# Optimization experiments

Hardware: AMD Instinct MI355X
Metric: run time of the kernel (lower is better)

Reference implementation:

```python
import jax, jax.numpy as jnp
import numpy as np
import math

NEG_INF = -1e9  # large negative used as masked-logit value (pre-scaling, as in the original)


def setup_inputs() -> dict:
    key = jax.random.key(0)
    k1, k2, k3 = jax.random.split(key, 3)
    bs, ql, kl, d = 8, 2048, 2048, 512
    return {
        "query": jax.random.normal(k1, (bs, ql, d), dtype=jnp.float32),
        "key": jax.random.normal(k2, (bs, kl, d), dtype=jnp.float32),
        "value": jax.random.normal(k3, (bs, kl, d), dtype=jnp.float32),
        "use_mask": 1,
        "cell_dim": 512,
    }


def reference(query, key, value, use_mask, cell_dim):
    bs, ql, d = query.shape[0], query.shape[1], value.shape[2]
    kl = key.shape[1]
    # [bs, ql, kl] raw scores
    mm = jnp.einsum("bqd,bkd->bqk", query, key)
    if use_mask:
        # mask positions where key index > query index (strictly future)
        q_idx = jnp.arange(ql)[:, None]
        k_idx = jnp.arange(kl)[None, :]
        mask = (k_idx > q_idx).astype(mm.dtype)  # [ql, kl]
        mm = mm + mask[None, :, :] * NEG_INF
    # log_softmax(...).exp() == softmax, computed stably in one pass
    w = jax.nn.softmax(mm / math.sqrt(cell_dim), axis=2)
    # weighted value aggregation (original broadcasts to [bs,ql,kl,d]; einsum fuses it)
    res = jnp.einsum("bqk,bkd->bqd", w, value)
    return res
```

## Files before the change

kernel.cpp:

```cpp
#include <hip/hip_runtime.h>
#include <math.h>

typedef __bf16 bf16x8 __attribute__((ext_vector_type(8)));
typedef float floatx4 __attribute__((ext_vector_type(4)));
typedef unsigned short ushort8_t __attribute__((ext_vector_type(8)));

#define BSZ 8
#define SEQ 2048
#define DIM 512
#define BKEY 32
#define BQ 128
#define NSLOT 70

__device__ __forceinline__ unsigned short f2bf(float f) {
    unsigned int u = __float_as_uint(f);
    u += 0x7fffu + ((u >> 16) & 1u);
    return (unsigned short)(u >> 16);
}
__device__ __forceinline__ float bf2f(unsigned short s) {
    return __uint_as_float(((unsigned int)s) << 16);
}

#define ASYNC16(g, l) __builtin_amdgcn_global_load_lds( \
    (const __attribute__((address_space(1))) unsigned int*)(g), \
    (__attribute__((address_space(3))) unsigned int*)(l), 16, 0, 0)

__global__ __launch_bounds__(256) void conv_k(const float* __restrict__ K,
                                              unsigned short* __restrict__ Kb) {
    size_t i = ((size_t)blockIdx.x * 256 + threadIdx.x) * 8;
    float4 a = *(const float4*)(K + i);
    float4 b = *(const float4*)(K + i + 4);
    ushort8_t u;
    u[0]=f2bf(a.x); u[1]=f2bf(a.y); u[2]=f2bf(a.z); u[3]=f2bf(a.w);
    u[4]=f2bf(b.x); u[5]=f2bf(b.y); u[6]=f2bf(b.z); u[7]=f2bf(b.w);
    *(ushort8_t*)(Kb + i) = u;
}

__global__ __launch_bounds__(256) void trans_v(const float* __restrict__ V,
                                               unsigned short* __restrict__ Vt) {
    __shared__ unsigned short T[BKEY][DIM + 8];
    const int bid = blockIdx.x;
    const int b = bid & 7, kb = bid >> 3;
    const float* src = V + ((size_t)b * SEQ + (size_t)kb * BKEY) * DIM;
    const int tid = threadIdx.x;
    #pragma unroll
    for (int i = 0; i < 16; ++i) {
        const int idx = i * 256 + tid;
        const int key = idx >> 7;
        const int d = (idx & 127) * 4;
        float4 x = *(const float4*)(src + (size_t)key * DIM + d);
        T[key][d]   = f2bf(x.x);
        T[key][d+1] = f2bf(x.y);
        T[key][d+2] = f2bf(x.z);
        T[key][d+3] = f2bf(x.w);
    }
    __syncthreads();
    unsigned short* dst = Vt + (size_t)(b * (SEQ / BKEY) + kb) * DIM * BKEY;
    #pragma unroll
    for (int i = 0; i < 8; ++i) {
        const int cidx = i * 256 + tid;
        const int d = cidx >> 2;
        const int kc = cidx & 3;
        ushort8_t v;
        #pragma unroll
        for (int k2 = 0; k2 < 8; ++k2) v[k2] = T[kc * 8 + k2][d];
        *(ushort8_t*)(dst + cidx * 8) = v;
    }
}


template <int SPLIT>
__global__ __launch_bounds__(512, 2)
void attn_fwd(const float* __restrict__ Q,
              const unsigned short* __restrict__ Kb,
              const unsigned short* __restrict__ Vt,
              unsigned short* __restrict__ PartO,
              float* __restrict__ Pml,
              float* __restrict__ O)
{
    __shared__ unsigned short Ksh[2][BKEY * DIM];
    __shared__ unsigned short Vsh[2][DIM * BKEY];
    __shared__ unsigned short Psh[8 * 16 * BKEY];

    const int tid  = threadIdx.x;
    const int lane = tid & 63;
    const int wv   = tid >> 6;
    const int ml   = lane & 15;
    const int quad = lane >> 4;

    const int bid = blockIdx.x;
    const int b   = bid & 7;
    const int j   = bid >> 3;
    int t, c;
    if (SPLIT) {
        t = 15; c = j;
        while (true) { const int cnt = (t + 2) >> 1; if (c < cnt) break; c -= cnt; --t; }
    } else { t = 15 - j; c = 0; }
    const int kt0 = c * 8;
    const int nk  = 4 * t + 4;
    const int kt1 = min(kt0 + 8, nk);
    const bool is_split = SPLIT && (t >= 2);
    const int q0 = t * BQ;
    const int kdiag = 4 * t;

    const float* Qb = Q + (size_t)b * SEQ * DIM;
    const unsigned short* Kbb = Kb + (size_t)b * SEQ * DIM;
    const unsigned short* Vtb = Vt + (size_t)b * SEQ * DIM;
    float* Ob = O + (size_t)b * SEQ * DIM;

    bf16x8 qf[16];
    {
        const float* qp = Qb + (size_t)(q0 + wv * 16 + ml) * DIM + quad * 8;
        #pragma unroll
        for (int kc = 0; kc < 16; ++kc) {
            float4 x = *(const float4*)(qp + kc * 32);
            float4 y = *(const float4*)(qp + kc * 32 + 4);
            union { bf16x8 v; unsigned short s[8]; } u;
            u.s[0]=f2bf(x.x); u.s[1]=f2bf(x.y); u.s[2]=f2bf(x.z); u.s[3]=f2bf(x.w);
            u.s[4]=f2bf(y.x); u.s[5]=f2bf(y.y); u.s[6]=f2bf(y.z); u.s[7]=f2bf(y.w);
            qf[kc] = u.v;
        }
    }
    asm volatile("" ::: "memory");

    floatx4 acc[32];
    #pragma unroll
    for (int i = 0; i < 32; ++i) acc[i] = (floatx4){0.f, 0.f, 0.f, 0.f};
    float mrun[4] = {-INFINITY, -INFINITY, -INFINITY, -INFINITY};
    float lrun[4] = {0.f, 0.f, 0.f, 0.f};

    const float CS = 1.4426950408889634f * 0.04419417382415922f;

    #define STAGE_K(buf_, kt_) do { \
        const unsigned short* Kt_ = Kbb + (size_t)(kt_) * (BKEY * DIM); \
        unsigned short* Kd_ = &Ksh[(buf_)][0]; \
        _Pragma("unroll") \
        for (int i_ = 0; i_ < 4; ++i_) { \
            const int ci_  = i_ * 512 + tid; \
            const int row_ = ci_ >> 6; \
            const int ch_  = (ci_ & 63) ^ (row_ & 7); \
            ASYNC16(Kt_ + (size_t)row_ * DIM + ch_ * 8, Kd_ + ci_ * 8); \
        } } while (0)
    #define STAGE_V(buf_, kt_) do { \
        const unsigned short* Vt_ = Vtb + (size_t)(kt_) * (DIM * BKEY); \
        unsigned short* Vd_ = &Vsh[(buf_)][0]; \
        _Pragma("unroll") \
        for (int i_ = 0; i_ < 4; ++i_) { \
            const int ci_ = i_ * 512 + tid; \
            const int d_  = ci_ >> 2; \
            const int kc_ = (ci_ & 3) ^ (d_ & 3); \
            ASYNC16(Vt_ + d_ * BKEY + kc_ * 8, Vd_ + ci_ * 8); \
        } } while (0)

    STAGE_K(0, kt0);
    STAGE_V(0, kt0);
    asm volatile("s_waitcnt vmcnt(4)" ::: "memory");
    __builtin_amdgcn_s_barrier();

    int cur = 0;
    for (int kt = kt0; kt < kt1; ++kt) {
        const int k0 = kt * BKEY;
        const bool havenxt = (kt + 1 < kt1);

        if (havenxt) STAGE_K(cur ^ 1, kt + 1);

        const unsigned short* Ks = &Ksh[cur][0];
        floatx4 s0 = (floatx4){0,0,0,0}, s1 = (floatx4){0,0,0,0};
        floatx4 s0b = (floatx4){0,0,0,0}, s1b = (floatx4){0,0,0,0};
        const int sw = ml & 7;
        __builtin_amdgcn_s_setprio(1);
        #pragma unroll
        for (int kc = 0; kc < 16; kc += 2) {
            const int ch0 = kc * 4 + quad, ch1 = (kc + 1) * 4 + quad;
            bf16x8 a0 = *(bf16x8*)&Ks[ml * DIM + ((ch0 ^ sw) << 3)];
            bf16x8 a1 = *(bf16x8*)&Ks[(16 + ml) * DIM + ((ch0 ^ sw) << 3)];
            bf16x8 b0 = *(bf16x8*)&Ks[ml * DIM + ((ch1 ^ sw) << 3)];
            bf16x8 b1 = *(bf16x8*)&Ks[(16 + ml) * DIM + ((ch1 ^ sw) << 3)];
            s0  = __builtin_amdgcn_mfma_f32_16x16x32_bf16(qf[kc],     a0, s0,  0, 0, 0);
            s1  = __builtin_amdgcn_mfma_f32_16x16x32_bf16(qf[kc],     a1, s1,  0, 0, 0);
            s0b = __builtin_amdgcn_mfma_f32_16x16x32_bf16(qf[kc + 1], b0, s0b, 0, 0, 0);
            s1b = __builtin_amdgcn_mfma_f32_16x16x32_bf16(qf[kc + 1], b1, s1b, 0, 0, 0);
        }
        __builtin_amdgcn_s_setprio(0);
        s0 = s0 + s0b;
        s1 = s1 + s1b;

        float z[2][4], pr[2][4], al[4], rs[4];
        if (kt >= kdiag) {
            #pragma unroll
            for (int r = 0; r < 4; ++r) {
                const int qg = q0 + wv * 16 + quad * 4 + r;
                z[0][r] = (k0 + ml > qg)      ? -INFINITY : s0[r] * CS;
                z[1][r] = (k0 + 16 + ml > qg) ? -INFINITY : s1[r] * CS;
            }
        } else {
            #pragma unroll
            for (int r = 0; r < 4; ++r) { z[0][r] = s0[r] * CS; z[1][r] = s1[r] * CS; }
        }
        #pragma unroll
        for (int r = 0; r < 4; ++r) {
            float v = fmaxf(z[0][r], z[1][r]);
            v = fmaxf(v, __shfl_xor(v, 1, 64));
            v = fmaxf(v, __shfl_xor(v, 2, 64));
            v = fmaxf(v, __shfl_xor(v, 4, 64));
            v = fmaxf(v, __shfl_xor(v, 8, 64));
            const float nm = fmaxf(mrun[r], v);
            al[r]   = __builtin_amdgcn_exp2f(mrun[r] - nm);
            mrun[r] = nm;
        }
        #pragma unroll
        for (int r = 0; r < 4; ++r) {
            pr[0][r] = __builtin_amdgcn_exp2f(z[0][r] - mrun[r]);
            pr[1][r] = __builtin_amdgcn_exp2f(z[1][r] - mrun[r]);
            float s = pr[0][r] + pr[1][r];
            s += __shfl_xor(s, 1, 64);
            s += __shfl_xor(s, 2, 64);
            s += __shfl_xor(s, 4, 64);
            s += __shfl_xor(s, 8, 64);
            rs[r] = s;
        }
        #pragma unroll
        for (int r = 0; r < 4; ++r) lrun[r] = lrun[r] * al[r] + rs[r];

        if (al[0] < 1.f || al[1] < 1.f || al[2] < 1.f || al[3] < 1.f) {
            #pragma unroll
            for (int nt = 0; nt < 32; ++nt) {
                acc[nt][0] *= al[0]; acc[nt][1] *= al[1];
                acc[nt][2] *= al[2]; acc[nt][3] *= al[3];
            }
        }

        unsigned short* Pw = &Psh[wv * (16 * BKEY)];
        #pragma unroll
        for (int nt = 0; nt < 2; ++nt) {
            #pragma unroll
            for (int r = 0; r < 4; ++r) {
                const int row = quad * 4 + r, col = nt * 16 + ml;
                Pw[row * BKEY + ((((col >> 3) ^ (row & 3)) << 3) | (col & 7))] = f2bf(pr[nt][r]);
            }
        }
        asm volatile("s_waitcnt lgkmcnt(0)" ::: "memory");
        bf16x8 pf = *(bf16x8*)&Pw[ml * BKEY + ((quad ^ (ml & 3)) << 3)];

        if (havenxt) { asm volatile("s_waitcnt vmcnt(4)" ::: "memory"); }
        else         { asm volatile("s_waitcnt vmcnt(0)" ::: "memory"); }
        __builtin_amdgcn_s_barrier();

        if (havenxt) STAGE_V(cur ^ 1, kt + 1);

        const unsigned short* Vs = &Vsh[cur][0];
        __builtin_amdgcn_s_setprio(1);
        #pragma unroll
        for (int nt = 0; nt < 32; ++nt) {
            const int drow = nt * 16 + ml;
            bf16x8 vf = *(bf16x8*)&Vs[drow * BKEY + ((quad ^ (drow & 3)) << 3)];
            acc[nt] = __builtin_amdgcn_mfma_f32_16x16x32_bf16(pf, vf, acc[nt], 0, 0, 0);
        }
        __builtin_amdgcn_s_setprio(0);

        if (havenxt) {
            asm volatile("s_waitcnt vmcnt(4)" ::: "memory");
            __builtin_amdgcn_s_barrier();
            cur ^= 1;
        }
    }
    #undef STAGE_K
    #undef STAGE_V

    if (!is_split) {
        float inv[4];
        #pragma unroll
        for (int r = 0; r < 4; ++r) inv[r] = 1.f / lrun[r];
        #pragma unroll
        for (int nt = 0; nt < 32; ++nt) {
            #pragma unroll
            for (int r = 0; r < 4; ++r) {
                const int row = q0 + wv * 16 + quad * 4 + r;
                Ob[(size_t)row * DIM + nt * 16 + ml] = acc[nt][r] * inv[r];
            }
        }
    } else {
        const size_t slot = (size_t)(b * NSLOT + j);
        unsigned short* po = PartO + slot * (BQ * DIM);
        #pragma unroll
        for (int nt = 0; nt < 32; ++nt) {
            #pragma unroll
            for (int r = 0; r < 4; ++r) {
                const int prow = wv * 16 + quad * 4 + r;
                po[prow * DIM + nt * 16 + ml] = f2bf(acc[nt][r]);
            }
        }
        if (ml == 0) {
            #pragma unroll
            for (int r = 0; r < 4; ++r) {
                const int prow = wv * 16 + quad * 4 + r;
                Pml[slot * 256 + prow * 2]     = mrun[r];
                Pml[slot * 256 + prow * 2 + 1] = lrun[r];
            }
        }
    }
}

__global__ __launch_bounds__(256)
void attn_merge(const unsigned short* __restrict__ PartO,
                const float* __restrict__ Pml,
                float* __restrict__ O)
{
    const int bid = blockIdx.x;
    const int b = bid & 7;
    const int u = bid >> 3;
    const int t = 2 + (u >> 2);
    const int rg = u & 3;
    const int nc = (t + 2) >> 1;
    int j0 = 0;
    for (int tp = 15; tp > t; --tp) j0 += (tp + 2) >> 1;

    const int r   = threadIdx.x >> 3;
    const int row = rg * 32 + r;
    const int d0  = (threadIdx.x & 7) * 64;

    float M = -INFINITY;
    for (int cc = 0; cc < nc; ++cc) {
        const size_t slot = (size_t)(b * NSLOT + j0 + cc);
        M = fmaxf(M, Pml[slot * 256 + row * 2]);
    }
    float L = 0.f;
    for (int cc = 0; cc < nc; ++cc) {
        const size_t slot = (size_t)(b * NSLOT + j0 + cc);
        L += Pml[slot * 256 + row * 2 + 1] *
             __builtin_amdgcn_exp2f(Pml[slot * 256 + row * 2] - M);
    }

    float o[64];
    #pragma unroll
    for (int i = 0; i < 64; ++i) o[i] = 0.f;
    for (int cc = 0; cc < nc; ++cc) {
        const size_t slot = (size_t)(b * NSLOT + j0 + cc);
        const float w = __builtin_amdgcn_exp2f(Pml[slot * 256 + row * 2] - M);
        const unsigned short* po = PartO + slot * (BQ * DIM) + (size_t)row * DIM + d0;
        #pragma unroll
        for (int i = 0; i < 8; ++i) {
            ushort8_t v = *(const ushort8_t*)(po + i * 8);
            #pragma unroll
            for (int k2 = 0; k2 < 8; ++k2) o[i * 8 + k2] += w * bf2f(v[k2]);
        }
    }
    const float invL = 1.f / L;
    float* out = O + ((size_t)b * SEQ + (size_t)t * BQ + row) * DIM + d0;
    #pragma unroll
    for (int i = 0; i < 16; ++i) {
        float4 v4 = { o[i*4] * invL, o[i*4+1] * invL, o[i*4+2] * invL, o[i*4+3] * invL };
        *(float4*)(out + i * 4) = v4;
    }
}

extern "C" void kernel_launch(void* const* d_in, const int* in_sizes, int n_in,
                              void* d_out, int out_size, void* d_ws, size_t ws_size,
                              hipStream_t stream) {
    const float* Q = (const float*)d_in[0];
    const float* K = (const float*)d_in[1];
    const float* V = (const float*)d_in[2];
    float* Out = (float*)d_out;

    const size_t elems = (size_t)BSZ * SEQ * DIM;
    unsigned short* Kb = (unsigned short*)d_ws;
    unsigned short* Vt = Kb + elems;
    unsigned short* PartO = Vt + elems;
    float* Pml = (float*)(PartO + (size_t)BSZ * NSLOT * BQ * DIM);

    const size_t need_split = 2 * elems * 2
                            + (size_t)BSZ * NSLOT * BQ * DIM * 2
                            + (size_t)BSZ * NSLOT * 256 * 4;
    conv_k<<<dim3(elems / 8 / 256), dim3(256), 0, stream>>>(K, Kb);
    trans_v<<<dim3(BSZ * (SEQ / BKEY)), dim3(256), 0, stream>>>(V, Vt);

    if (ws_size >= need_split) {
        attn_fwd<1><<<dim3(BSZ * 72), dim3(512), 0, stream>>>(Q, Kb, Vt, PartO, Pml, Out);
        attn_merge<<<dim3(BSZ * 14 * 4), dim3(256), 0, stream>>>(PartO, Pml, Out);
    } else {
        attn_fwd<0><<<dim3(BSZ * 16), dim3(512), 0, stream>>>(Q, Kb, Vt, PartO, Pml, Out);
    }
}
```

Measured before the change: 338.5 us.

## Process two key tiles per iteration and skip small running-max rescales

Each loop iteration now handles two 32-key tiles (64 keys) using both shared buffers, so softmax reductions, barriers and the P write/read run once per 64 keys instead of once per 32. Staging moves from ping-pong overlap to loading the next pair after compute, which can expose load latency because no double buffering remains. The running-max update now only rescales when the new max exceeds the old by more than 8 (log2 units), cutting accumulator rescales at the cost of a looser bound on exponent range. This assumes an even number of tiles per chunk.

Result: slower. 419.9 us (+24.1%).

```diff
diff --git a/kernel.cpp b/kernel.cpp
--- a/kernel.cpp
+++ b/kernel.cpp
@@ -80,7 +80,7 @@
 {
     __shared__ unsigned short Ksh[2][BKEY * DIM];
     __shared__ unsigned short Vsh[2][DIM * BKEY];
-    __shared__ unsigned short Psh[8 * 16 * BKEY];
+    __shared__ unsigned short Psh[8 * 16 * 64];
 
     const int tid  = threadIdx.x;
     const int lane = tid & 63;
@@ -152,75 +152,82 @@
             ASYNC16(Vt_ + d_ * BKEY + kc_ * 8, Vd_ + ci_ * 8); \
         } } while (0)
 
-    STAGE_K(0, kt0);
-    STAGE_V(0, kt0);
-    asm volatile("s_waitcnt vmcnt(4)" ::: "memory");
+    STAGE_K(0, kt0); STAGE_K(1, kt0 + 1);
+    STAGE_V(0, kt0); STAGE_V(1, kt0 + 1);
+    asm volatile("s_waitcnt vmcnt(8)" ::: "memory");
     __builtin_amdgcn_s_barrier();
 
-    int cur = 0;
-    for (int kt = kt0; kt < kt1; ++kt) {
+    for (int kt = kt0; kt < kt1; kt += 2) {
         const int k0 = kt * BKEY;
-        const bool havenxt = (kt + 1 < kt1);
-
-        if (havenxt) STAGE_K(cur ^ 1, kt + 1);
-
-        const unsigned short* Ks = &Ksh[cur][0];
-        floatx4 s0 = (floatx4){0,0,0,0}, s1 = (floatx4){0,0,0,0};
-        floatx4 s0b = (floatx4){0,0,0,0}, s1b = (floatx4){0,0,0,0};
+        const bool havenxt = (kt + 2 < kt1);
+
+        const unsigned short* KsA = &Ksh[0][0];
+        const unsigned short* KsB = &Ksh[1][0];
+        floatx4 s[4];
+        #pragma unroll
+        for (int i = 0; i < 4; ++i) s[i] = (floatx4){0.f, 0.f, 0.f, 0.f};
         const int sw = ml & 7;
         __builtin_amdgcn_s_setprio(1);
         #pragma unroll
-        for (int kc = 0; kc < 16; kc += 2) {
-            const int ch0 = kc * 4 + quad, ch1 = (kc + 1) * 4 + quad;
-            bf16x8 a0 = *(bf16x8*)&Ks[ml * DIM + ((ch0 ^ sw) << 3)];
-            bf16x8 a1 = *(bf16x8*)&Ks[(16 + ml) * DIM + ((ch0 ^ sw) << 3)];
-            bf16x8 b0 = *(bf16x8*)&Ks[ml * DIM + ((ch1 ^ sw) << 3)];
-            bf16x8 b1 = *(bf16x8*)&Ks[(16 + ml) * DIM + ((ch1 ^ sw) << 3)];
-            s0  = __builtin_amdgcn_mfma_f32_16x16x32_bf16(qf[kc],     a0, s0,  0, 0, 0);
-            s1  = __builtin_amdgcn_mfma_f32_16x16x32_bf16(qf[kc],     a1, s1,  0, 0, 0);
-            s0b = __builtin_amdgcn_mfma_f32_16x16x32_bf16(qf[kc + 1], b0, s0b, 0, 0, 0);
-            s1b = __builtin_amdgcn_mfma_f32_16x16x32_bf16(qf[kc + 1], b1, s1b, 0, 0, 0);
+        for (int kc = 0; kc < 16; ++kc) {
+            const int off = ((kc * 4 + quad) ^ sw) << 3;
+            bf16x8 a0 = *(bf16x8*)&KsA[ml * DIM + off];
+            bf16x8 a1 = *(bf16x8*)&KsA[(16 + ml) * DIM + off];
+            bf16x8 b0 = *(bf16x8*)&KsB[ml * DIM + off];
+            bf16x8 b1 = *(bf16x8*)&KsB[(16 + ml) * DIM + off];
+            s[0] = __builtin_amdgcn_mfma_f32_16x16x32_bf16(qf[kc], a0, s[0], 0, 0, 0);
+            s[1] = __builtin_amdgcn_mfma_f32_16x16x32_bf16(qf[kc], a1, s[1], 0, 0, 0);
+            s[2] = __builtin_amdgcn_mfma_f32_16x16x32_bf16(qf[kc], b0, s[2], 0, 0, 0);
+            s[3] = __builtin_amdgcn_mfma_f32_16x16x32_bf16(qf[kc], b1, s[3], 0, 0, 0);
         }
         __builtin_amdgcn_s_setprio(0);
-        s0 = s0 + s0b;
-        s1 = s1 + s1b;
-
-        float z[2][4], pr[2][4], al[4], rs[4];
-        if (kt >= kdiag) {
+
+        asm volatile("" ::: "memory");
+        __builtin_amdgcn_s_barrier();
+        if (havenxt) { STAGE_K(0, kt + 2); STAGE_K(1, kt + 3); }
+
+        if (kt + 1 >= kdiag) {
             #pragma unroll
             for (int r = 0; r < 4; ++r) {
                 const int qg = q0 + wv * 16 + quad * 4 + r;
-                z[0][r] = (k0 + ml > qg)      ? -INFINITY : s0[r] * CS;
-                z[1][r] = (k0 + 16 + ml > qg) ? -INFINITY : s1[r] * CS;
+                s[0][r] = (k0 + ml > qg)      ? -INFINITY : s[0][r] * CS;
+                s[1][r] = (k0 + 16 + ml > qg) ? -INFINITY : s[1][r] * CS;
+                s[2][r] = (k0 + 32 + ml > qg) ? -INFINITY : s[2][r] * CS;
+                s[3][r] = (k0 + 48 + ml > qg) ? -INFINITY : s[3][r] * CS;
             }
         } else {
             #pragma unroll
-            for (int r = 0; r < 4; ++r) { z[0][r] = s0[r] * CS; z[1][r] = s1[r] * CS; }
-        }
+            for (int r = 0; r < 4; ++r) {
+                s[0][r] *= CS; s[1][r] *= CS; s[2][r] *= CS; s[3][r] *= CS;
+            }
+        }
+
+        float al[4];
         #pragma unroll
         for (int r = 0; r < 4; ++r) {
-            float v = fmaxf(z[0][r], z[1][r]);
+            float v = fmaxf(fmaxf(s[0][r], s[1][r]), fmaxf(s[2][r], s[3][r]));
             v = fmaxf(v, __shfl_xor(v, 1, 64));
             v = fmaxf(v, __shfl_xor(v, 2, 64));
             v = fmaxf(v, __shfl_xor(v, 4, 64));
             v = fmaxf(v, __shfl_xor(v, 8, 64));
-            const float nm = fmaxf(mrun[r], v);
-            al[r]   = __builtin_amdgcn_exp2f(mrun[r] - nm);
-            mrun[r] = nm;
+            const float d = v - mrun[r];
+            const bool up = d > 8.0f;
+            al[r]   = up ? __builtin_amdgcn_exp2f(-d) : 1.0f;
+            mrun[r] = up ? v : mrun[r];
         }
         #pragma unroll
         for (int r = 0; r < 4; ++r) {
-            pr[0][r] = __builtin_amdgcn_exp2f(z[0][r] - mrun[r]);
-            pr[1][r] = __builtin_amdgcn_exp2f(z[1][r] - mrun[r]);
-            float s = pr[0][r] + pr[1][r];
-            s += __shfl_xor(s, 1, 64);
-            s += __shfl_xor(s, 2, 64);
-            s += __shfl_xor(s, 4, 64);
-            s += __shfl_xor(s, 8, 64);
-            rs[r] = s;
-        }
-        #pragma unroll
-        for (int r = 0; r < 4; ++r) lrun[r] = lrun[r] * al[r] + rs[r];
+            s[0][r] = __builtin_amdgcn_exp2f(s[0][r] - mrun[r]);
+            s[1][r] = __builtin_amdgcn_exp2f(s[1][r] - mrun[r]);
+            s[2][r] = __builtin_amdgcn_exp2f(s[2][r] - mrun[r]);
+            s[3][r] = __builtin_amdgcn_exp2f(s[3][r] - mrun[r]);
+            float rs = (s[0][r] + s[1][r]) + (s[2][r] + s[3][r]);
+            rs += __shfl_xor(rs, 1, 64);
+            rs += __shfl_xor(rs, 2, 64);
+            rs += __shfl_xor(rs, 4, 64);
+            rs += __shfl_xor(rs, 8, 64);
+            lrun[r] = lrun[r] * al[r] + rs;
+        }
 
         if (al[0] < 1.f || al[1] < 1.f || al[2] < 1.f || al[3] < 1.f) {
             #pragma unroll
@@ -230,38 +237,43 @@
             }
         }
 
-        unsigned short* Pw = &Psh[wv * (16 * BKEY)];
-        #pragma unroll
-        for (int nt = 0; nt < 2; ++nt) {
+        unsigned short* Pw = &Psh[wv * (16 * 64)];
+        #pragma unroll
+        for (int nt = 0; nt < 4; ++nt) {
             #pragma unroll
             for (int r = 0; r < 4; ++r) {
                 const int row = quad * 4 + r, col = nt * 16 + ml;
-                Pw[row * BKEY + ((((col >> 3) ^ (row & 3)) << 3) | (col & 7))] = f2bf(pr[nt][r]);
+                Pw[row * 64 + ((((col >> 3) ^ (row & 7)) << 3) | (col & 7))] = f2bf(s[nt][r]);
             }
         }
         asm volatile("s_waitcnt lgkmcnt(0)" ::: "memory");
-        bf16x8 pf = *(bf16x8*)&Pw[ml * BKEY + ((quad ^ (ml & 3)) << 3)];
-
-        if (havenxt) { asm volatile("s_waitcnt vmcnt(4)" ::: "memory"); }
+        bf16x8 pf0 = *(bf16x8*)&Pw[ml * 64 + ((quad ^ (ml & 7)) << 3)];
+        bf16x8 pf1 = *(bf16x8*)&Pw[ml * 64 + (((4 + quad) ^ (ml & 7)) << 3)];
+
+        if (havenxt) { asm volatile("s_waitcnt vmcnt(8)" ::: "memory"); }
         else         { asm volatile("s_waitcnt vmcnt(0)" ::: "memory"); }
         __builtin_amdgcn_s_barrier();
 
-        if (havenxt) STAGE_V(cur ^ 1, kt + 1);
-
-        const unsigned short* Vs = &Vsh[cur][0];
+        const unsigned short* VsA = &Vsh[0][0];
+        const unsigned short* VsB = &Vsh[1][0];
         __builtin_amdgcn_s_setprio(1);
         #pragma unroll
         for (int nt = 0; nt < 32; ++nt) {
             const int drow = nt * 16 + ml;
-            bf16x8 vf = *(bf16x8*)&Vs[drow * BKEY + ((quad ^ (drow & 3)) << 3)];
-            acc[nt] = __builtin_amdgcn_mfma_f32_16x16x32_bf16(pf, vf, acc[nt], 0, 0, 0);
+            const int off = drow * BKEY + ((quad ^ (drow & 3)) << 3);
+            bf16x8 vfA = *(bf16x8*)&VsA[off];
+            bf16x8 vfB = *(bf16x8*)&VsB[off];
+            acc[nt] = __builtin_amdgcn_mfma_f32_16x16x32_bf16(pf0, vfA, acc[nt], 0, 0, 0);
+            acc[nt] = __builtin_amdgcn_mfma_f32_16x16x32_bf16(pf1, vfB, acc[nt], 0, 0, 0);
         }
         __builtin_amdgcn_s_setprio(0);
 
         if (havenxt) {
-            asm volatile("s_waitcnt vmcnt(4)" ::: "memory");
+            asm volatile("" ::: "memory");
             __builtin_amdgcn_s_barrier();
-            cur ^= 1;
+            STAGE_V(0, kt + 2); STAGE_V(1, kt + 3);
+            asm volatile("s_waitcnt vmcnt(8)" ::: "memory");
+            __builtin_amdgcn_s_barrier();
         }
     }
     #undef STAGE_K
```
